# Performance work log

Measured on AMD Instinct MI355X. Metric: run time of the kernel, lower is better.

## Reference

```python
import jax, jax.numpy as jnp
import numpy as np

EPS = 1e-06
NMAX = 0.85

def _pad_edge(x):
    # replicate-pad H and W by 1 on each side
    return jnp.pad(x, ((0, 0), (0, 0), (1, 1), (1, 1)), mode='edge')

def _avg_and_gradsq(x):
    # 4-neighbor average (cross stencil / 4) and centered-difference |grad|^2
    xp = _pad_edge(x)
    up_ = xp[:, :, :-2, 1:-1]
    dn_ = xp[:, :, 2:, 1:-1]
    lf_ = xp[:, :, 1:-1, :-2]
    rt_ = xp[:, :, 1:-1, 2:]
    avg = 0.25 * (up_ + dn_ + lf_ + rt_)
    gx = 0.5 * (rt_ - lf_)
    gy = 0.5 * (dn_ - up_)
    return avg, gx * gx + gy * gy

def setup_inputs() -> dict:
    key = jax.random.key(0)
    ks = jax.random.split(key, 5)
    shp = (16, 3, 512, 512)
    u = jax.random.uniform(ks[0], shp, dtype=jnp.float32)
    v = jax.random.uniform(ks[1], shp, dtype=jnp.float32)
    u0 = jax.random.uniform(ks[2], shp, dtype=jnp.float32)
    p = jax.random.uniform(ks[3], shp, dtype=jnp.float32)
    q = jax.random.uniform(ks[4], shp, dtype=jnp.float32)
    params = dict(
        alpha=jnp.float32(0.45), beta=jnp.float32(0.35),
        kappa=jnp.float32(0.14), lam=jnp.float32(0.12), omega=jnp.float32(0.78))
    return {"u": u, "v": v, "u0": u0, "p": p, "q": q, **params}

def reference(u, v, u0, p, q, alpha, beta, kappa, lam, omega):
    u_safe = jnp.maximum(u, EPS)
    v_safe = jnp.maximum(v, EPS)
    N_u = jnp.minimum(p * jnp.power(v_safe, alpha), NMAX)
    N_v = jnp.minimum(q * jnp.power(u_safe, beta), NMAX)

    u_avg, grad_sq_u = _avg_and_gradsq(u)
    v_avg, grad_sq_v = _avg_and_gradsq(v)

    inv_k2 = 1.0 / (kappa * kappa)
    c_edge_u = jnp.exp(-grad_sq_u * inv_k2)
    c_edge_v = jnp.exp(-grad_sq_v * inv_k2)

    u_smooth = u_avg + N_u * 0.25
    v_smooth = v_avg + N_v * 0.25
    u_cand = c_edge_u * u_smooth + (1.0 - c_edge_u) * u
    v_cand = c_edge_v * v_smooth + (1.0 - c_edge_v) * v

    u_new = (1.0 - omega) * u + omega * ((1.0 - lam) * u_cand + lam * u0)
    v_new = (1.0 - omega) * v + omega * ((1.0 - lam) * v_cand + lam * u0)
    return (u_new, v_new)
```

## Files before the change

### kernel.cpp

```cpp
#include <hip/hip_runtime.h>

namespace {

constexpr int H = 512;
constexpr int W = 512;
constexpr float EPSV   = 1e-6f;
constexpr float NMAXV  = 0.85f;
constexpr float LOG2E  = 1.4426950408889634f;

typedef float f4v __attribute__((ext_vector_type(4)));

__device__ __forceinline__ float fexp2(float x) {
#if __has_builtin(__builtin_amdgcn_exp2f)
    return __builtin_amdgcn_exp2f(x);
#else
    return exp2f(x);
#endif
}
__device__ __forceinline__ float flog2(float x) {
#if __has_builtin(__builtin_amdgcn_logf)
    return __builtin_amdgcn_logf(x);
#else
    return log2f(x);
#endif
}

__device__ __forceinline__ void unpack(const float4 v, float o[4]) {
    o[0] = v.x; o[1] = v.y; o[2] = v.z; o[3] = v.w;
}

__global__ __launch_bounds__(256) void lef_kernel(
    const float* __restrict__ u,  const float* __restrict__ v,
    const float* __restrict__ u0, const float* __restrict__ p,
    const float* __restrict__ q,
    const float* __restrict__ s_alpha, const float* __restrict__ s_beta,
    const float* __restrict__ s_kappa, const float* __restrict__ s_lam,
    const float* __restrict__ s_omega,
    float* __restrict__ out_u, float* __restrict__ out_v)
{
    const float alpha = s_alpha[0];
    const float beta  = s_beta[0];
    const float kappa = s_kappa[0];
    const float lam   = s_lam[0];
    const float omega = s_omega[0];
    const float nk2    = (1.0f / (kappa * kappa)) * LOG2E;
    const float w_cand = omega * (1.0f - lam);
    const float w_u0   = omega * lam;
    const float w_self = 1.0f - omega;

    const int tid   = blockIdx.x * 256 + threadIdx.x;
    const int xq    = tid & 127;
    const int rest  = tid >> 7;
    const int yb    = rest & 127;
    const int plane = rest >> 7;
    const int x0    = xq << 2;
    const int y0    = yb << 2;
    const int pb    = plane * (H * W);

    int ro[6];
    ro[0] = pb + ((y0 > 0) ? y0 - 1 : 0) * W + x0;
    ro[1] = pb + y0 * W + x0;
    ro[2] = ro[1] + W;
    ro[3] = ro[2] + W;
    ro[4] = ro[3] + W;
    ro[5] = pb + ((y0 + 4 < H) ? y0 + 4 : H - 1) * W + x0;

    float ur[6][4], vr[6][4];
#pragma unroll
    for (int i = 0; i < 6; ++i) unpack(*(const float4*)(u + ro[i]), ur[i]);
#pragma unroll
    for (int i = 0; i < 6; ++i) unpack(*(const float4*)(v + ro[i]), vr[i]);

    float u0r[4][4], pr[4][4], qr[4][4];
#pragma unroll
    for (int i = 0; i < 4; ++i) unpack(*(const float4*)(u0 + ro[i + 1]), u0r[i]);
#pragma unroll
    for (int i = 0; i < 4; ++i) unpack(*(const float4*)(p + ro[i + 1]), pr[i]);
#pragma unroll
    for (int i = 0; i < 4; ++i) unpack(*(const float4*)(q + ro[i + 1]), qr[i]);

    const bool le = (x0 == 0);
    const bool re = (x0 == W - 4);
    float ulf[4], urt[4], vlf[4], vrt[4];
#pragma unroll
    for (int i = 0; i < 4; ++i) {
        const int rc = ro[i + 1];
        ulf[i] = le ? ur[i + 1][0] : u[rc - 1];
        urt[i] = re ? ur[i + 1][3] : u[rc + 4];
        vlf[i] = le ? vr[i + 1][0] : v[rc - 1];
        vrt[i] = re ? vr[i + 1][3] : v[rc + 4];
    }

#pragma unroll
    for (int i = 0; i < 4; ++i) {
        const float* uu = ur[i];
        const float* uc = ur[i + 1];
        const float* ud = ur[i + 2];
        const float* vu = vr[i];
        const float* vc = vr[i + 1];
        const float* vd = vr[i + 2];
        const float ul[4] = {ulf[i], uc[0], uc[1], uc[2]};
        const float ur_[4] = {uc[1], uc[2], uc[3], urt[i]};
        const float vl[4] = {vlf[i], vc[0], vc[1], vc[2]};
        const float vr_[4] = {vc[1], vc[2], vc[3], vrt[i]};

        f4v ou, ov;
#pragma unroll
        for (int j = 0; j < 4; ++j) {
            const float uavg = 0.25f * (uu[j] + ud[j] + ul[j] + ur_[j]);
            const float ugx = 0.5f * (ur_[j] - ul[j]);
            const float ugy = 0.5f * (ud[j] - uu[j]);
            const float ugsq = ugx * ugx + ugy * ugy;
            const float vavg = 0.25f * (vu[j] + vd[j] + vl[j] + vr_[j]);
            const float vgx = 0.5f * (vr_[j] - vl[j]);
            const float vgy = 0.5f * (vd[j] - vu[j]);
            const float vgsq = vgx * vgx + vgy * vgy;

            const float u_safe = fmaxf(uc[j], EPSV);
            const float v_safe = fmaxf(vc[j], EPSV);
            const float N_u = fminf(pr[i][j] * fexp2(alpha * flog2(v_safe)), NMAXV);
            const float N_v = fminf(qr[i][j] * fexp2(beta  * flog2(u_safe)), NMAXV);
            const float ce_u = fexp2(-ugsq * nk2);
            const float ce_v = fexp2(-vgsq * nk2);
            const float u_sm = uavg + N_u * 0.25f;
            const float v_sm = vavg + N_v * 0.25f;
            const float u_cand = ce_u * u_sm + (1.0f - ce_u) * uc[j];
            const float v_cand = ce_v * v_sm + (1.0f - ce_v) * vc[j];
            ou[j] = w_self * uc[j] + w_cand * u_cand + w_u0 * u0r[i][j];
            ov[j] = w_self * vc[j] + w_cand * v_cand + w_u0 * u0r[i][j];
        }
        __builtin_nontemporal_store(ou, (f4v*)(out_u + ro[i + 1]));
        __builtin_nontemporal_store(ov, (f4v*)(out_v + ro[i + 1]));
    }
}

}

extern "C" void kernel_launch(void* const* d_in, const int* in_sizes, int n_in,
                              void* d_out, int out_size, void* d_ws, size_t ws_size,
                              hipStream_t stream)
{
    const float* u  = (const float*)d_in[0];
    const float* v  = (const float*)d_in[1];
    const float* u0 = (const float*)d_in[2];
    const float* p  = (const float*)d_in[3];
    const float* q  = (const float*)d_in[4];
    const float* s_alpha = (const float*)d_in[5];
    const float* s_beta  = (const float*)d_in[6];
    const float* s_kappa = (const float*)d_in[7];
    const float* s_lam   = (const float*)d_in[8];
    const float* s_omega = (const float*)d_in[9];

    const int n_elems = in_sizes[0];
    const int nplanes = n_elems / (H * W);
    float* out_u = (float*)d_out;
    float* out_v = (float*)d_out + n_elems;

    const int threads = nplanes * (H / 4) * (W / 4);
    const int block = 256;
    const int grid  = threads / block;

    lef_kernel<<<grid, block, 0, stream>>>(u, v, u0, p, q,
                                           s_alpha, s_beta, s_kappa, s_lam, s_omega,
                                           out_u, out_v);
}
```

Before: 60.86 us.

## Map each wavefront to one full row and share halo columns via lane shuffles

```diff
diff --git a/kernel.cpp b/kernel.cpp
--- a/kernel.cpp
+++ b/kernel.cpp
@@ -25,8 +25,11 @@
 #endif
 }
 
-__device__ __forceinline__ void unpack(const float4 v, float o[4]) {
-    o[0] = v.x; o[1] = v.y; o[2] = v.z; o[3] = v.w;
+__device__ __forceinline__ void load8(const float* __restrict__ a, int off, float o[8]) {
+    const float4 x = *(const float4*)(a + off);
+    const float4 y = *(const float4*)(a + off + 4);
+    o[0] = x.x; o[1] = x.y; o[2] = x.z; o[3] = x.w;
+    o[4] = y.x; o[5] = y.y; o[6] = y.z; o[7] = y.w;
 }
 
 __global__ __launch_bounds__(256) void lef_kernel(
@@ -49,89 +52,73 @@
     const float w_self = 1.0f - omega;
 
     const int tid   = blockIdx.x * 256 + threadIdx.x;
-    const int xq    = tid & 127;
-    const int rest  = tid >> 7;
-    const int yb    = rest & 127;
-    const int plane = rest >> 7;
-    const int x0    = xq << 2;
-    const int y0    = yb << 2;
-    const int pb    = plane * (H * W);
+    const int lane  = threadIdx.x & 63;
+    const int wid   = tid >> 6;
+    const int y     = wid & (H - 1);
+    const int plane = wid >> 9;
+    const int xo    = lane << 3;
 
-    int ro[6];
-    ro[0] = pb + ((y0 > 0) ? y0 - 1 : 0) * W + x0;
-    ro[1] = pb + y0 * W + x0;
-    ro[2] = ro[1] + W;
-    ro[3] = ro[2] + W;
-    ro[4] = ro[3] + W;
-    ro[5] = pb + ((y0 + 4 < H) ? y0 + 4 : H - 1) * W + x0;
+    const int pb = plane * (H * W);
+    const int rc = pb + y * W + xo;
+    const int rm = pb + ((y > 0)     ? y - 1 : 0)     * W + xo;
+    const int rp = pb + ((y < H - 1) ? y + 1 : H - 1) * W + xo;
 
-    float ur[6][4], vr[6][4];
+    float uu[8], uc[8], ud[8], vu[8], vc[8], vd[8];
+    load8(u, rm, uu);  load8(u, rc, uc);  load8(u, rp, ud);
+    load8(v, rm, vu);  load8(v, rc, vc);  load8(v, rp, vd);
+    float u0c[8], pc[8], qc[8];
+    load8(u0, rc, u0c);
+    load8(p,  rc, pc);
+    load8(q,  rc, qc);
+
+    float ulf0 = __shfl_up(uc[7], 1);
+    float vlf0 = __shfl_up(vc[7], 1);
+    float urt7 = __shfl_down(uc[0], 1);
+    float vrt7 = __shfl_down(vc[0], 1);
+    ulf0 = (lane == 0)  ? uc[0] : ulf0;
+    vlf0 = (lane == 0)  ? vc[0] : vlf0;
+    urt7 = (lane == 63) ? uc[7] : urt7;
+    vrt7 = (lane == 63) ? vc[7] : vrt7;
+
+    const float ulf[8] = {ulf0, uc[0], uc[1], uc[2], uc[3], uc[4], uc[5], uc[6]};
+    const float urt[8] = {uc[1], uc[2], uc[3], uc[4], uc[5], uc[6], uc[7], urt7};
+    const float vlf[8] = {vlf0, vc[0], vc[1], vc[2], vc[3], vc[4], vc[5], vc[6]};
+    const float vrt[8] = {vc[1], vc[2], vc[3], vc[4], vc[5], vc[6], vc[7], vrt7};
+
+    float ou[8], ov[8];
 #pragma unroll
-    for (int i = 0; i < 6; ++i) unpack(*(const float4*)(u + ro[i]), ur[i]);
-#pragma unroll
-    for (int i = 0; i < 6; ++i) unpack(*(const float4*)(v + ro[i]), vr[i]);
+    for (int j = 0; j < 8; ++j) {
+        const float uavg = 0.25f * (uu[j] + ud[j] + ulf[j] + urt[j]);
+        const float ugx  = 0.5f * (urt[j] - ulf[j]);
+        const float ugy  = 0.5f * (ud[j] - uu[j]);
+        const float ugsq = ugx * ugx + ugy * ugy;
+        const float vavg = 0.25f * (vu[j] + vd[j] + vlf[j] + vrt[j]);
+        const float vgx  = 0.5f * (vrt[j] - vlf[j]);
+        const float vgy  = 0.5f * (vd[j] - vu[j]);
+        const float vgsq = vgx * vgx + vgy * vgy;
 
-    float u0r[4][4], pr[4][4], qr[4][4];
-#pragma unroll
-    for (int i = 0; i < 4; ++i) unpack(*(const float4*)(u0 + ro[i + 1]), u0r[i]);
-#pragma unroll
-    for (int i = 0; i < 4; ++i) unpack(*(const float4*)(p + ro[i + 1]), pr[i]);
-#pragma unroll
-    for (int i = 0; i < 4; ++i) unpack(*(const float4*)(q + ro[i + 1]), qr[i]);
-
-    const bool le = (x0 == 0);
-    const bool re = (x0 == W - 4);
-    float ulf[4], urt[4], vlf[4], vrt[4];
-#pragma unroll
-    for (int i = 0; i < 4; ++i) {
-        const int rc = ro[i + 1];
-        ulf[i] = le ? ur[i + 1][0] : u[rc - 1];
-        urt[i] = re ? ur[i + 1][3] : u[rc + 4];
-        vlf[i] = le ? vr[i + 1][0] : v[rc - 1];
-        vrt[i] = re ? vr[i + 1][3] : v[rc + 4];
+        const float u_safe = fmaxf(uc[j], EPSV);
+        const float v_safe = fmaxf(vc[j], EPSV);
+        const float N_u = fminf(pc[j] * fexp2(alpha * flog2(v_safe)), NMAXV);
+        const float N_v = fminf(qc[j] * fexp2(beta  * flog2(u_safe)), NMAXV);
+        const float ce_u = fexp2(-ugsq * nk2);
+        const float ce_v = fexp2(-vgsq * nk2);
+        const float u_sm = uavg + N_u * 0.25f;
+        const float v_sm = vavg + N_v * 0.25f;
+        const float u_cand = ce_u * u_sm + (1.0f - ce_u) * uc[j];
+        const float v_cand = ce_v * v_sm + (1.0f - ce_v) * vc[j];
+        ou[j] = w_self * uc[j] + w_cand * u_cand + w_u0 * u0c[j];
+        ov[j] = w_self * vc[j] + w_cand * v_cand + w_u0 * u0c[j];
     }
 
-#pragma unroll
-    for (int i = 0; i < 4; ++i) {
-        const float* uu = ur[i];
-        const float* uc = ur[i + 1];
-        const float* ud = ur[i + 2];
-        const float* vu = vr[i];
-        const float* vc = vr[i + 1];
-        const float* vd = vr[i + 2];
-        const float ul[4] = {ulf[i], uc[0], uc[1], uc[2]};
-        const float ur_[4] = {uc[1], uc[2], uc[3], urt[i]};
-        const float vl[4] = {vlf[i], vc[0], vc[1], vc[2]};
-        const float vr_[4] = {vc[1], vc[2], vc[3], vrt[i]};
-
-        f4v ou, ov;
-#pragma unroll
-        for (int j = 0; j < 4; ++j) {
-            const float uavg = 0.25f * (uu[j] + ud[j] + ul[j] + ur_[j]);
-            const float ugx = 0.5f * (ur_[j] - ul[j]);
-            const float ugy = 0.5f * (ud[j] - uu[j]);
-            const float ugsq = ugx * ugx + ugy * ugy;
-            const float vavg = 0.25f * (vu[j] + vd[j] + vl[j] + vr_[j]);
-            const float vgx = 0.5f * (vr_[j] - vl[j]);
-            const float vgy = 0.5f * (vd[j] - vu[j]);
-            const float vgsq = vgx * vgx + vgy * vgy;
-
-            const float u_safe = fmaxf(uc[j], EPSV);
-            const float v_safe = fmaxf(vc[j], EPSV);
-            const float N_u = fminf(pr[i][j] * fexp2(alpha * flog2(v_safe)), NMAXV);
-            const float N_v = fminf(qr[i][j] * fexp2(beta  * flog2(u_safe)), NMAXV);
-            const float ce_u = fexp2(-ugsq * nk2);
-            const float ce_v = fexp2(-vgsq * nk2);
-            const float u_sm = uavg + N_u * 0.25f;
-            const float v_sm = vavg + N_v * 0.25f;
-            const float u_cand = ce_u * u_sm + (1.0f - ce_u) * uc[j];
-            const float v_cand = ce_v * v_sm + (1.0f - ce_v) * vc[j];
-            ou[j] = w_self * uc[j] + w_cand * u_cand + w_u0 * u0r[i][j];
-            ov[j] = w_self * vc[j] + w_cand * v_cand + w_u0 * u0r[i][j];
-        }
-        __builtin_nontemporal_store(ou, (f4v*)(out_u + ro[i + 1]));
-        __builtin_nontemporal_store(ov, (f4v*)(out_v + ro[i + 1]));
-    }
+    const f4v ou_lo = {ou[0], ou[1], ou[2], ou[3]};
+    const f4v ou_hi = {ou[4], ou[5], ou[6], ou[7]};
+    const f4v ov_lo = {ov[0], ov[1], ov[2], ov[3]};
+    const f4v ov_hi = {ov[4], ov[5], ov[6], ov[7]};
+    __builtin_nontemporal_store(ou_lo, (f4v*)(out_u + rc));
+    __builtin_nontemporal_store(ou_hi, (f4v*)(out_u + rc + 4));
+    __builtin_nontemporal_store(ov_lo, (f4v*)(out_v + rc));
+    __builtin_nontemporal_store(ov_hi, (f4v*)(out_v + rc + 4));
 }
 
 }
@@ -156,7 +143,7 @@
     float* out_u = (float*)d_out;
     float* out_v = (float*)d_out + n_elems;
 
-    const int threads = nplanes * (H / 4) * (W / 4);
+    const int threads = nplanes * H * 64;
     const int block = 256;
     const int grid  = threads / block;
 
```

Measured after the change: 109.1 us. 79.3% more time.
